# Kernel tuning notes

Measured on AMD Instinct MI355X. Metric: run time of the kernel, lower is better.

The kernel has to match this reference:

```python
import jax, jax.numpy as jnp
import numpy as np

# ---- static skeleton structure (SMPL 24-joint, 23-edge kinematic tree) ----
SMPL_EDGES = [[0,1],[0,2],[0,3],[1,4],[2,5],[3,6],[4,7],[5,8],[6,9],[7,10],
              [8,11],[9,12],[9,13],[9,14],[12,15],[13,16],[14,17],[16,18],
              [17,19],[18,20],[19,21],[20,22],[21,23]]
KERNEL, STRIDE, PAD, DIST = 15, 2, 7, 1

def _edge_dist(edges):
    E = len(edges)
    m = np.full((E, E), 1e6)
    np.fill_diagonal(m, 0.0)
    for i, a in enumerate(edges):
        for j, b in enumerate(edges):
            if i != j and set(a) & set(b):
                m[i, j] = 1.0
    for k in range(E):  # Floyd-Warshall on the edge adjacency graph
        m = np.minimum(m, m[:, k:k+1] + m[k:k+1, :])
    return m

def _find_neighbor(edges, d, n_global):
    m = _edge_dist(edges); E = len(edges)
    nb = [list(np.nonzero(m[i] <= d)[0]) for i in range(E)]
    gp = list(nb[0])  # edges near root edge (keeps deep-motion-editing's known quirk)
    g_ids = [E + k for k in range(n_global)]
    for i in gp:
        nb[i].extend(g_ids)
    for _ in range(n_global):
        nb.append(gp + g_ids)
    return nb

def _find_seqs(edges):
    deg = {}
    for a, b in edges:
        deg[a] = deg.get(a, 0) + 1
        deg[b] = deg.get(b, 0) + 1
    seqs = []
    def rec(j, seq):
        if deg.get(j, 0) > 2 and j != 0:
            seqs.append(seq); seq = []
        if deg.get(j, 0) == 1:
            seqs.append(seq); return
        for idx, (a, b) in enumerate(edges):
            if a == j:
                rec(b, seq + [idx])
    rec(0, [])
    return seqs

def _pooling(edges, last_pool, global_ids):
    pools, new_edges = [], []
    for seq in _find_seqs(edges):
        if last_pool:
            pools.append(seq); continue
        if len(seq) % 2 == 1:
            pools.append([seq[0]]); new_edges.append(edges[seq[0]]); seq = seq[1:]
        for i in range(0, len(seq), 2):
            pools.append([seq[i], seq[i+1]])
            new_edges.append([edges[seq[i]][0], edges[seq[i+1]][1]])
    pools.append(list(global_ids))
    return pools, new_edges

def _conv_mask(nb, in_per, out_per):
    N = len(nb)
    mask = np.zeros((N*out_per, N*in_per, 1), np.float32)
    for i, ns in enumerate(nb):
        for j in ns:
            mask[i*out_per:(i+1)*out_per, j*in_per:(j+1)*in_per, 0] = 1.0
    return mask

def _pool_matrix(pools, n_nodes, cpe):
    W = np.zeros((len(pools)*cpe, n_nodes*cpe), np.float32)
    c = np.arange(cpe)
    for i, grp in enumerate(pools):
        for j in grp:
            W[i*cpe + c, j*cpe + c] = 1.0 / len(grp)
    return W

E0 = len(SMPL_EDGES)
N0 = E0 + 2  # 23 edges + global position node + root-velocity node (the '+4' channels)
MASK0 = jnp.asarray(_conv_mask(_find_neighbor(SMPL_EDGES, DIST, 2), 4, 8))  # (200,100,1)
_pools0, EDGES1 = _pooling(SMPL_EDGES, False, [E0, E0 + 1])
P0 = jnp.asarray(_pool_matrix(_pools0, N0, 8))  # (112,200)
N1 = len(EDGES1) + 1
MASK1 = jnp.asarray(_conv_mask(_find_neighbor(EDGES1, DIST, 1), 8, 16))  # (224,112,1)
_pools1, _ = _pooling(EDGES1, True, [N1 - 1])
P1 = jnp.asarray(_pool_matrix(_pools1, N1, 16))  # (112,224)

IN0, OUT0 = 4 * N0, 8 * N0    # 100, 200
IN1, OUT1 = 8 * N1, 16 * N1   # 112, 224
B, T_IN = 64, 2047            # 2048 frames after zero-frame append


def _skel_conv(x, w, b, mask):
    # masked Conv1d (skeleton-sparse weights), stride 2, zero padding 7, k=15
    y = jax.lax.conv_general_dilated(x, w * mask, window_strides=(STRIDE,),
                                     padding=[(PAD, PAD)],
                                     dimension_numbers=('NCH', 'OIH', 'NCH'))
    return y + b[None, :, None]


def _forward(x, w0, b0, w1, b1):
    # x: (B, T, C); append one zero frame on time dim, then to (B, C, T+1)
    out = jnp.concatenate([x, jnp.zeros_like(x[:, :1, :])], axis=1)
    out = out.transpose(0, 2, 1)
    out = jax.nn.relu(jnp.einsum('pc,bct->bpt', P0, _skel_conv(out, w0, b0, MASK0)))
    out = jax.nn.relu(jnp.einsum('pc,bct->bpt', P1, _skel_conv(out, w1, b1, MASK1)))
    return out  # (B, 112, (T+1)//4)


def setup_inputs() -> dict:
    key = jax.random.key(0)
    k = jax.random.split(key, 5)
    s = 0.05
    return {
        'x':  jax.random.normal(k[0], (B, T_IN, IN0), jnp.float32),
        'w0': jax.random.normal(k[1], (OUT0, IN0, KERNEL), jnp.float32) * s,
        'b0': jax.random.normal(k[2], (OUT0,), jnp.float32) * s,
        'w1': jax.random.normal(k[3], (OUT1, IN1, KERNEL), jnp.float32) * s,
        'b1': jax.random.normal(k[4], (OUT1,), jnp.float32) * s,
    }


def reference(x, w0, b0, w1, b1):
    return _forward(x, w0, b0, w1, b1)
```

## Files before the change

### kernel.cpp

```cpp
#include <hip/hip_runtime.h>


#define OFF_A2  107520u
#define OFF_BF0 322560u
#define OFF_BF1 323008u
#define OFF_Y0  323584u

typedef unsigned int uint32;
typedef __attribute__((ext_vector_type(8))) short bs8;
typedef __attribute__((ext_vector_type(4))) float f32x4;
union U8 { uint4 u; bs8 s; };

__constant__ int c_pool0_len[14] = {2,2,2,2,1,2,2,1,2,2,1,2,2,2};
__constant__ int c_pool0_mem[14][2] = {{0,3},{6,9},{1,4},{7,10},{2,2},{5,8},{11,14},{12,12},
                                       {15,17},{19,21},{13,13},{16,18},{20,22},{23,24}};
__constant__ unsigned c_nbm0[25] = {
 0x180000Fu,0x1800017u,0x1800027u,0x1800049u,0x92u,0x124u,0x248u,0x490u,
 0x3920u,0x240u,0x480u,0x7900u,0xB900u,0x13900u,0x4800u,0x29000u,
 0x52000u,0xA8000u,0x150000u,0x2A0000u,0x540000u,0x280000u,0x500000u,
 0x180000Fu,0x180000Fu
};
__constant__ int c_pool1_len[7] = {2,2,2,1,3,3,1};
__constant__ int c_pool1_mem[7][3] = {{0,1,1},{2,3,3},{4,5,5},{6,6,6},{7,8,9},{10,11,12},{13,13,13}};
__constant__ unsigned c_nbm1[14] = {
 0x2017u,0x2003u,0x201Du,0xCu,0x2035u,0x4F0u,0x4E0u,0x5E0u,
 0x380u,0x300u,0xCE0u,0x1C00u,0x1800u,0x2017u
};
__constant__ int c_g1p[7][2] = {{0,13},{1,3},{2,4},{5,6},{7,10},{8,11},{9,12}};
__constant__ int c_U1[7][8] = {
 {0,1,2,3,6,23,24,25},
 {3,4,6,7,9,10,25,25},
 {0,1,2,4,5,7,23,24},
 {2,5,8,11,12,13,14,25},
 {8,11,12,13,15,16,25,25},
 {12,13,15,16,17,18,19,20},
 {17,18,19,20,21,22,25,25}};
__constant__ int c_U2[7][8] = {
 {0,1,2,4,13,14,14,14},
 {0,2,3,4,13,14,14,14},
 {0,2,4,5,6,7,10,13},
 {5,6,7,10,14,14,14,14},
 {5,6,7,8,9,10,14,14},
 {5,6,7,10,11,12,14,14},
 {0,1,2,4,13,14,14,14}};
__constant__ unsigned c_pk1a[7] = {0xC0301000u,0xC8483018u,0xB8281000u,0x70604010u,
                                   0xC8786040u,0x98887860u,0xC8A89888u};
__constant__ unsigned c_pk1b[7] = {0xC8B81808u,0xC8503820u,0xC0382008u,0xC8685828u,
                                   0xC8806858u,0xA0908068u,0xC8B0A090u};
__constant__ unsigned c_pk2[7][2] = {
 {0x40201000u,0xE0E0E0D0u},{0x40302000u,0xE0E0E0D0u},{0x50402000u,0xD0A07060u},
 {0xA0706050u,0xE0E0E0E0u},{0x80706050u,0xE0E0A090u},{0xA0706050u,0xE0E0C0B0u},
 {0x40201000u,0xE0E0E0D0u}};

__device__ __forceinline__ uint32 f2bf(float v) {
  uint32 u = __float_as_uint(v);
  return (u + 0x7fffu + ((u >> 16) & 1u)) >> 16;
}

__global__ void prep_fused_weights(const float* __restrict__ w0, const float* __restrict__ b0,
                                   const float* __restrict__ w1, const float* __restrict__ b1,
                                   char* __restrict__ wsb) {
  int t = blockIdx.x * blockDim.x + threadIdx.x;
  if (t < 6720) {
    int lane = t & 63;
    int r = t >> 6;
    int k = r % 15, g = r / 15;
    int m = lane & 15, h = lane >> 4;
    int pool = (m < 8) ? c_g1p[g][0] : c_g1p[g][1];
    int c = m & 7;
    int L = c_pool0_len[pool];
    float inv = 1.f / (float)L;
    uint32 us[8];
#pragma unroll
    for (int j = 0; j < 8; ++j) {
      int node = c_U1[g][2 * h + (j >> 2)];
      int ci = j & 3;
      float v = 0.f;
      if (node < 25) {
        for (int jj = 0; jj < L; ++jj) {
          int mem = c_pool0_mem[pool][jj];
          if ((c_nbm0[mem] >> node) & 1u)
            v += w0[(mem * 8 + c) * 1500 + (node * 4 + ci) * 15 + k];
        }
        v *= inv;
      }
      us[j] = f2bf(v);
    }
    uint4 o = make_uint4(us[0] | (us[1] << 16), us[2] | (us[3] << 16),
                         us[4] | (us[5] << 16), us[6] | (us[7] << 16));
    reinterpret_cast<uint4*>(wsb)[t] = o;
  } else if (t < 6720 + 13440) {
    int t2 = t - 6720;
    int lane = t2 & 63;
    int r = t2 >> 6;
    int k = r % 15;
    int r2 = r / 15;
    int ks = r2 & 1, p = r2 >> 1;
    int c = lane & 15, h = lane >> 4;
    int node = c_U2[p][ks * 4 + h];
    int L = c_pool1_len[p];
    float inv = 1.f / (float)L;
    uint32 us[8];
#pragma unroll
    for (int j = 0; j < 8; ++j) {
      float v = 0.f;
      if (node < 14) {
        for (int jj = 0; jj < L; ++jj) {
          int mem = c_pool1_mem[p][jj];
          if ((c_nbm1[mem] >> node) & 1u)
            v += w1[(mem * 16 + c) * 1680 + (node * 8 + j) * 15 + k];
        }
        v *= inv;
      }
      us[j] = f2bf(v);
    }
    uint4 o = make_uint4(us[0] | (us[1] << 16), us[2] | (us[3] << 16),
                         us[4] | (us[5] << 16), us[6] | (us[7] << 16));
    reinterpret_cast<uint4*>(wsb + OFF_A2)[t2] = o;
  } else if (t < 6720 + 13440 + 112) {
    int p = t - (6720 + 13440);
    int i = p >> 3, c = p & 7;
    int L = c_pool0_len[i];
    float v = 0.f;
    for (int jj = 0; jj < L; ++jj) v += b0[c_pool0_mem[i][jj] * 8 + c];
    reinterpret_cast<float*>(wsb + OFF_BF0)[p] = v / (float)L;
  } else if (t < 6720 + 13440 + 224) {
    int p = t - (6720 + 13440 + 112);
    int i = p >> 4, c = p & 15;
    int L = c_pool1_len[i];
    float v = 0.f;
    for (int jj = 0; jj < L; ++jj) v += b1[c_pool1_mem[i][jj] * 16 + c];
    reinterpret_cast<float*>(wsb + OFF_BF1)[p] = v / (float)L;
  }
}

__global__ __launch_bounds__(448, 7) void conv_stage1(const float* __restrict__ x,
                                                      const char* __restrict__ wsb,
                                                      char* __restrict__ y0b) {
  __shared__ __align__(16) unsigned char xs[141 * 232];
  const int tid = threadIdx.x;
  const int b = blockIdx.y;
  const int t0 = blockIdx.x << 6;
  const int g0 = 2 * t0 - 7;
  const float* __restrict__ xb = x + (size_t)b * (2047 * 100);

  for (int e = tid; e < 141 * 32; e += 448) {
    int f = e >> 5, q = e & 31;
    if (q >= 29) continue;
    uint2 w = make_uint2(0u, 0u);
    int gt = g0 + f;
    if (q < 25 && (unsigned)gt < 2047u) {
      float4 v = *reinterpret_cast<const float4*>(xb + gt * 100 + 4 * q);
      w.x = f2bf(v.x) | (f2bf(v.y) << 16);
      w.y = f2bf(v.z) | (f2bf(v.w) << 16);
    }
    *reinterpret_cast<uint2*>(xs + f * 232 + q * 8) = w;
  }
  __syncthreads();

  const int lane = tid & 63;
  const int g = tid >> 6;
  const int m16 = lane & 15, h = lane >> 4;
  const uint32 offA = (c_pk1a[g] >> (8 * h)) & 255u;
  const uint32 offB = (c_pk1b[g] >> (8 * h)) & 255u;
  const uint4* __restrict__ A1p = reinterpret_cast<const uint4*>(wsb);

  f32x4 acc[4];
#pragma unroll
  for (int nt = 0; nt < 4; ++nt) acc[nt] = (f32x4)0.f;

#pragma unroll 1
  for (int k = 0; k < 15; ++k) {
    U8 a; a.u = A1p[(g * 15 + k) * 64 + lane];
    const uint32 base = (uint32)((2 * m16 + k) * 232);
#pragma unroll
    for (int nt = 0; nt < 4; ++nt) {
      const uint32 ad = base + nt * (32 * 232);
      uint2 lo = *reinterpret_cast<const uint2*>(xs + ad + offA);
      uint2 hi = *reinterpret_cast<const uint2*>(xs + ad + offB);
      U8 bfr; bfr.u = make_uint4(lo.x, lo.y, hi.x, hi.y);
      acc[nt] = __builtin_amdgcn_mfma_f32_16x16x32_bf16(a.s, bfr.s, acc[nt], 0, 0, 0);
    }
  }

  const int pa = c_g1p[g][0], pb = c_g1p[g][1];
  const int chbase = (h < 2) ? (pa * 8 + 4 * h) : (pb * 8 + 4 * (h - 2));
  const float4 bv = *reinterpret_cast<const float4*>(wsb + OFF_BF0 + chbase * 4);
  __syncthreads();
#pragma unroll
  for (int nt = 0; nt < 4; ++nt) {
    float o0 = fmaxf(acc[nt][0] + bv.x, 0.f);
    float o1 = fmaxf(acc[nt][1] + bv.y, 0.f);
    float o2 = fmaxf(acc[nt][2] + bv.z, 0.f);
    float o3 = fmaxf(acc[nt][3] + bv.w, 0.f);
    uint2 wpk = make_uint2(f2bf(o0) | (f2bf(o1) << 16), f2bf(o2) | (f2bf(o3) << 16));
    *reinterpret_cast<uint2*>(xs + (nt * 16 + m16) * 232 + chbase * 2) = wpk;
  }
  __syncthreads();
  for (int e = tid; e < 1024; e += 448) {
    int row = e >> 4, q = e & 15;
    if (q >= 14) continue;
    uint2 a = *reinterpret_cast<const uint2*>(xs + row * 232 + q * 16);
    uint2 d = *reinterpret_cast<const uint2*>(xs + row * 232 + q * 16 + 8);
    *reinterpret_cast<uint4*>(y0b + (size_t)(b * 1024 + t0 + row) * 224 + q * 16) =
        make_uint4(a.x, a.y, d.x, d.y);
  }
}

__global__ __launch_bounds__(448, 7) void conv_stage2(const char* __restrict__ wsb,
                                                      const char* __restrict__ y0b,
                                                      float* __restrict__ out) {
  __shared__ __align__(16) unsigned char xs[80 * 256];
  const int tid = threadIdx.x;
  const int b = blockIdx.y;
  const int t0 = blockIdx.x << 5;
  const int g0 = 2 * t0 - 7;
  const char* __restrict__ yb = y0b + (size_t)b * (1024 * 224);

  for (int e = tid; e < 77 * 16; e += 448) {
    int f = e >> 4, q = e & 15;
    uint4 v = make_uint4(0u, 0u, 0u, 0u);
    int gt = g0 + f;
    if (q < 14 && (unsigned)gt < 1024u)
      v = *reinterpret_cast<const uint4*>(yb + (size_t)gt * 224 + q * 16);
    int pr = (f >> 1) + (f & 1) * 40;
    *reinterpret_cast<uint4*>(xs + pr * 256 + ((q * 16) ^ ((pr & 7) << 4))) = v;
  }
  __syncthreads();

  const int lane = tid & 63;
  const int p = tid >> 6;
  const int m16 = lane & 15, h = lane >> 4;
  const uint4* __restrict__ A2p = reinterpret_cast<const uint4*>(wsb + OFF_A2);

  f32x4 acc[2];
  acc[0] = (f32x4)0.f; acc[1] = (f32x4)0.f;

#pragma unroll 1
  for (int ks = 0; ks < 2; ++ks) {
    const uint32 noff = (c_pk2[p][ks] >> (8 * h)) & 255u;
#pragma unroll 1
    for (int k = 0; k < 15; ++k) {
      U8 a; a.u = A2p[((p * 2 + ks) * 15 + k) * 64 + lane];
      const int prk = (k >> 1) + (k & 1) * 40;
#pragma unroll
      for (int nt = 0; nt < 2; ++nt) {
        int pr = nt * 16 + m16 + prk;
        U8 bfr;
        bfr.u = *reinterpret_cast<const uint4*>(xs + pr * 256 + (noff ^ ((pr & 7) << 4)));
        acc[nt] = __builtin_amdgcn_mfma_f32_16x16x32_bf16(a.s, bfr.s, acc[nt], 0, 0, 0);
      }
    }
  }

  const float4 bv = *reinterpret_cast<const float4*>(wsb + OFF_BF1 + (p * 16 + 4 * h) * 4);
#pragma unroll
  for (int nt = 0; nt < 2; ++nt) {
    size_t obase = ((size_t)b * 112 + p * 16 + 4 * h) * 512 + t0 + nt * 16 + m16;
    out[obase]        = fmaxf(acc[nt][0] + bv.x, 0.f);
    out[obase + 512]  = fmaxf(acc[nt][1] + bv.y, 0.f);
    out[obase + 1024] = fmaxf(acc[nt][2] + bv.z, 0.f);
    out[obase + 1536] = fmaxf(acc[nt][3] + bv.w, 0.f);
  }
}

extern "C" void kernel_launch(void* const* d_in, const int* in_sizes, int n_in,
                              void* d_out, int out_size, void* d_ws, size_t ws_size,
                              hipStream_t stream) {
  const float* x  = (const float*)d_in[0];
  const float* w0 = (const float*)d_in[1];
  const float* b0 = (const float*)d_in[2];
  const float* w1 = (const float*)d_in[3];
  const float* b1 = (const float*)d_in[4];
  char* wsb = (char*)d_ws;
  float* out = (float*)d_out;

  prep_fused_weights<<<80, 256, 0, stream>>>(w0, b0, w1, b1, wsb);
  conv_stage1<<<dim3(16, 64), 448, 0, stream>>>(x, wsb, wsb + OFF_Y0);
  conv_stage2<<<dim3(16, 64), 448, 0, stream>>>(wsb, wsb + OFF_Y0, out);
}
```

Measured before the change: 61.28 us.

## Prefetch MFMA weight fragments into registers before staging, swizzle stage-1 LDS

Both conv kernels now load all per-wave weight fragments from global memory into registers at kernel start, before the input tile is staged into shared memory, so the weight fetch latency overlaps the staging loop. The K loops are fully unrolled with precomputed swizzled addresses. Stage 1 pads LDS rows to 256 bytes and applies an XOR swizzle to cut bank conflicts on the B-fragment reads and the output writeback. The cost is much higher register pressure (15 or 30 uint4 fragments per lane), which may reduce occupancy under the 448x7 launch bounds or cause spills.

```diff
diff --git a/kernel.cpp b/kernel.cpp
--- a/kernel.cpp
+++ b/kernel.cpp
@@ -137,13 +137,24 @@
 __global__ __launch_bounds__(448, 7) void conv_stage1(const float* __restrict__ x,
                                                       const char* __restrict__ wsb,
                                                       char* __restrict__ y0b) {
-  __shared__ __align__(16) unsigned char xs[141 * 232];
+  __shared__ __align__(16) unsigned char xs[141 * 256];
   const int tid = threadIdx.x;
+  const int lane = tid & 63;
+  const int g = tid >> 6;
+  const int m16 = lane & 15, h = lane >> 4;
   const int b = blockIdx.y;
   const int t0 = blockIdx.x << 6;
   const int g0 = 2 * t0 - 7;
+
+  const uint4* __restrict__ A1p = reinterpret_cast<const uint4*>(wsb) + g * 960 + lane;
+  U8 a[15];
+#pragma unroll
+  for (int k = 0; k < 15; ++k) a[k].u = A1p[k * 64];
+  const int pa = c_g1p[g][0], pb = c_g1p[g][1];
+  const int chbase = (h < 2) ? (pa * 8 + 4 * h) : (pb * 8 + 4 * (h - 2));
+  const float4 bv = *reinterpret_cast<const float4*>(wsb + OFF_BF0 + chbase * 4);
+
   const float* __restrict__ xb = x + (size_t)b * (2047 * 100);
-
   for (int e = tid; e < 141 * 32; e += 448) {
     int f = e >> 5, q = e & 31;
     if (q >= 29) continue;
@@ -154,38 +165,31 @@
       w.x = f2bf(v.x) | (f2bf(v.y) << 16);
       w.y = f2bf(v.z) | (f2bf(v.w) << 16);
     }
-    *reinterpret_cast<uint2*>(xs + f * 232 + q * 8) = w;
-  }
-  __syncthreads();
-
-  const int lane = tid & 63;
-  const int g = tid >> 6;
-  const int m16 = lane & 15, h = lane >> 4;
+    *reinterpret_cast<uint2*>(xs + f * 256 + ((q * 8) ^ (((f >> 1) & 7) << 3))) = w;
+  }
+  __syncthreads();
+
   const uint32 offA = (c_pk1a[g] >> (8 * h)) & 255u;
   const uint32 offB = (c_pk1b[g] >> (8 * h)) & 255u;
-  const uint4* __restrict__ A1p = reinterpret_cast<const uint4*>(wsb);
 
   f32x4 acc[4];
 #pragma unroll
   for (int nt = 0; nt < 4; ++nt) acc[nt] = (f32x4)0.f;
 
-#pragma unroll 1
+#pragma unroll
   for (int k = 0; k < 15; ++k) {
-    U8 a; a.u = A1p[(g * 15 + k) * 64 + lane];
-    const uint32 base = (uint32)((2 * m16 + k) * 232);
+    const uint32 sw = (uint32)(((m16 + (k >> 1)) & 7) << 3);
+    const uint32 a0 = offA ^ sw, a1 = offB ^ sw;
+    const unsigned char* base = xs + (2 * m16 + k) * 256;
 #pragma unroll
     for (int nt = 0; nt < 4; ++nt) {
-      const uint32 ad = base + nt * (32 * 232);
-      uint2 lo = *reinterpret_cast<const uint2*>(xs + ad + offA);
-      uint2 hi = *reinterpret_cast<const uint2*>(xs + ad + offB);
+      uint2 lo = *reinterpret_cast<const uint2*>(base + nt * 8192 + a0);
+      uint2 hi = *reinterpret_cast<const uint2*>(base + nt * 8192 + a1);
       U8 bfr; bfr.u = make_uint4(lo.x, lo.y, hi.x, hi.y);
-      acc[nt] = __builtin_amdgcn_mfma_f32_16x16x32_bf16(a.s, bfr.s, acc[nt], 0, 0, 0);
-    }
-  }
-
-  const int pa = c_g1p[g][0], pb = c_g1p[g][1];
-  const int chbase = (h < 2) ? (pa * 8 + 4 * h) : (pb * 8 + 4 * (h - 2));
-  const float4 bv = *reinterpret_cast<const float4*>(wsb + OFF_BF0 + chbase * 4);
+      acc[nt] = __builtin_amdgcn_mfma_f32_16x16x32_bf16(a[k].s, bfr.s, acc[nt], 0, 0, 0);
+    }
+  }
+
   __syncthreads();
 #pragma unroll
   for (int nt = 0; nt < 4; ++nt) {
@@ -194,16 +198,18 @@
     float o2 = fmaxf(acc[nt][2] + bv.z, 0.f);
     float o3 = fmaxf(acc[nt][3] + bv.w, 0.f);
     uint2 wpk = make_uint2(f2bf(o0) | (f2bf(o1) << 16), f2bf(o2) | (f2bf(o3) << 16));
-    *reinterpret_cast<uint2*>(xs + (nt * 16 + m16) * 232 + chbase * 2) = wpk;
+    int row = nt * 16 + m16;
+    *reinterpret_cast<uint2*>(xs + row * 256 + ((chbase * 2) ^ ((row & 7) << 3))) = wpk;
   }
   __syncthreads();
   for (int e = tid; e < 1024; e += 448) {
     int row = e >> 4, q = e & 15;
     if (q >= 14) continue;
-    uint2 a = *reinterpret_cast<const uint2*>(xs + row * 232 + q * 16);
-    uint2 d = *reinterpret_cast<const uint2*>(xs + row * 232 + q * 16 + 8);
+    uint32 sw = (uint32)((row & 7) << 3);
+    uint2 av = *reinterpret_cast<const uint2*>(xs + row * 256 + ((q * 16) ^ sw));
+    uint2 dv = *reinterpret_cast<const uint2*>(xs + row * 256 + ((q * 16 + 8) ^ sw));
     *reinterpret_cast<uint4*>(y0b + (size_t)(b * 1024 + t0 + row) * 224 + q * 16) =
-        make_uint4(a.x, a.y, d.x, d.y);
+        make_uint4(av.x, av.y, dv.x, dv.y);
   }
 }
 
@@ -212,11 +218,20 @@
                                                       float* __restrict__ out) {
   __shared__ __align__(16) unsigned char xs[80 * 256];
   const int tid = threadIdx.x;
+  const int lane = tid & 63;
+  const int p = tid >> 6;
+  const int m16 = lane & 15, h = lane >> 4;
   const int b = blockIdx.y;
   const int t0 = blockIdx.x << 5;
   const int g0 = 2 * t0 - 7;
+
+  const uint4* __restrict__ A2p = reinterpret_cast<const uint4*>(wsb + OFF_A2) + p * 1920 + lane;
+  U8 a[30];
+#pragma unroll
+  for (int kk = 0; kk < 30; ++kk) a[kk].u = A2p[kk * 64];
+  const float4 bv = *reinterpret_cast<const float4*>(wsb + OFF_BF1 + (p * 16 + 4 * h) * 4);
+
   const char* __restrict__ yb = y0b + (size_t)b * (1024 * 224);
-
   for (int e = tid; e < 77 * 16; e += 448) {
     int f = e >> 4, q = e & 15;
     uint4 v = make_uint4(0u, 0u, 0u, 0u);
@@ -228,32 +243,26 @@
   }
   __syncthreads();
 
-  const int lane = tid & 63;
-  const int p = tid >> 6;
-  const int m16 = lane & 15, h = lane >> 4;
-  const uint4* __restrict__ A2p = reinterpret_cast<const uint4*>(wsb + OFF_A2);
-
   f32x4 acc[2];
   acc[0] = (f32x4)0.f; acc[1] = (f32x4)0.f;
-
-#pragma unroll 1
+  const uint32 mbase = (uint32)(m16 * 256);
+
+#pragma unroll
   for (int ks = 0; ks < 2; ++ks) {
     const uint32 noff = (c_pk2[p][ks] >> (8 * h)) & 255u;
-#pragma unroll 1
+#pragma unroll
     for (int k = 0; k < 15; ++k) {
-      U8 a; a.u = A2p[((p * 2 + ks) * 15 + k) * 64 + lane];
-      const int prk = (k >> 1) + (k & 1) * 40;
-#pragma unroll
-      for (int nt = 0; nt < 2; ++nt) {
-        int pr = nt * 16 + m16 + prk;
-        U8 bfr;
-        bfr.u = *reinterpret_cast<const uint4*>(xs + pr * 256 + (noff ^ ((pr & 7) << 4)));
-        acc[nt] = __builtin_amdgcn_mfma_f32_16x16x32_bf16(a.s, bfr.s, acc[nt], 0, 0, 0);
-      }
-    }
-  }
-
-  const float4 bv = *reinterpret_cast<const float4*>(wsb + OFF_BF1 + (p * 16 + 4 * h) * 4);
+      const uint32 sw = (uint32)(((m16 + (k >> 1)) & 7) << 4);
+      const uint32 ab = mbase + (noff ^ sw);
+      const int imm = ((k >> 1) + (k & 1) * 40) * 256;
+      U8 b0f, b1f;
+      b0f.u = *reinterpret_cast<const uint4*>(xs + ab + imm);
+      b1f.u = *reinterpret_cast<const uint4*>(xs + ab + imm + 4096);
+      acc[0] = __builtin_amdgcn_mfma_f32_16x16x32_bf16(a[ks * 15 + k].s, b0f.s, acc[0], 0, 0, 0);
+      acc[1] = __builtin_amdgcn_mfma_f32_16x16x32_bf16(a[ks * 15 + k].s, b1f.s, acc[1], 0, 0, 0);
+    }
+  }
+
 #pragma unroll
   for (int nt = 0; nt < 2; ++nt) {
     size_t obase = ((size_t)b * 112 + p * 16 + 4 * h) * 512 + t0 + nt * 16 + m16;
```

After: 107.9 us. 76.1% more time.
